# Kernel optimization log

Measured on AMD Instinct MI355X. Metric: run time of the kernel, lower is better.

The kernel has to match this reference:

```python
import jax, jax.numpy as jnp
import numpy as np

N = 50000        # nodes
E = 800000       # edges
D_IN = 128       # input feature dim (== 2*hidden)
H = 64           # hidden_dim
G = 64           # graphs in batch
BN_EPS = 1e-5


def setup_inputs() -> dict:
    key = jax.random.key(0)
    ks = jax.random.split(key, 8)
    x = jax.random.normal(ks[0], (N, D_IN), jnp.float32)
    edge_index = jax.random.randint(ks[1], (2, E), 0, N, dtype=jnp.int32)
    edge_attribute = jax.random.normal(ks[2], (E,), jnp.float32)
    batch = jnp.sort(jax.random.randint(ks[3], (N,), 0, G, dtype=jnp.int32))
    # 7 GIN layers; all first linears are [D_IN=2H -> H]
    W1 = jax.random.normal(ks[4], (7, D_IN, H), jnp.float32) * (1.0 / np.sqrt(D_IN))
    bn1_g = jnp.ones((7, H), jnp.float32)
    bn1_b = jnp.zeros((7, H), jnp.float32)
    # layers 0..5 second linear [H -> 2H] + BN
    W2 = jax.random.normal(ks[5], (6, H, 2 * H), jnp.float32) * (1.0 / np.sqrt(H))
    bn2_g = jnp.ones((6, 2 * H), jnp.float32)
    bn2_b = jnp.zeros((6, 2 * H), jnp.float32)
    # layer 6 second linear [H -> 2], no BN
    W_last = jax.random.normal(ks[6], (H, 2), jnp.float32) * (1.0 / np.sqrt(H))
    eps = jnp.zeros((7,), jnp.float32)  # train_eps=True, init 0
    return dict(x=x, edge_index=edge_index, edge_attribute=edge_attribute,
                batch=batch, W1=W1, bn1_g=bn1_g, bn1_b=bn1_b, W2=W2,
                bn2_g=bn2_g, bn2_b=bn2_b, W_last=W_last, eps=eps)


def _bn(h, g, b):
    # training-mode BatchNorm1d over node axis, biased variance
    mu = h.mean(0)
    var = h.var(0)
    return g * (h - mu) * jax.lax.rsqrt(var + BN_EPS) + b


def reference(x, edge_index, edge_attribute, batch, W1, bn1_g, bn1_b, W2,
              bn2_g, bn2_b, W_last, eps):
    src, dst = edge_index[0], edge_index[1]
    for i in range(7):
        # GIN aggregation: sum of neighbor features (edge_attribute unused)
        agg = jax.ops.segment_sum(x[src], dst, num_segments=N)
        h = (1.0 + eps[i]) * x + agg
        h = jax.nn.relu(_bn(h @ W1[i], bn1_g[i], bn1_b[i]))
        if i < 6:
            h = _bn(h @ W2[i], bn2_g[i], bn2_b[i])
        else:
            h = h @ W_last
        # F.dropout treated as identity (deterministic eval); then ReLU
        x = jax.nn.relu(h)
    # global_mean_pool over graphs
    counts = jax.ops.segment_sum(jnp.ones((N,), x.dtype), batch, num_segments=G)
    sums = jax.ops.segment_sum(x, batch, num_segments=G)
    return sums / jnp.maximum(counts, 1.0)[:, None]
```

## Files before the change

kernel.cpp:

```cpp
#include <hip/hip_runtime.h>
#include <hip/hip_fp16.h>

#define NN 50000
#define EE 800000
#define GG 64
#define BNEPS 1e-5f

typedef _Float16 f16x8 __attribute__((ext_vector_type(8)));
typedef float f32x4 __attribute__((ext_vector_type(4)));

__device__ inline float2 h2f(unsigned int u) {
    __half2 h = __builtin_bit_cast(__half2, u);
    return __half22float2(h);
}
__device__ inline unsigned int f2h(float a, float b) {
    __half2 h = __float22half2_rn(make_float2(a, b));
    return __builtin_bit_cast(unsigned int, h);
}
__device__ inline __half2 relu2(__half2 v) {
    const __half z = __float2half(0.f);
    return __halves2half2(__hmax(__low2half(v), z), __hmax(__high2half(v), z));
}


__global__ void hist_kernel(const int* __restrict__ ei, int* __restrict__ deg) {
    int e = blockIdx.x * 256 + threadIdx.x;
    if (e < EE) atomicAdd(&deg[ei[EE + e]], 1);
}

__global__ void scan1_kernel(const int* __restrict__ deg, int* __restrict__ offs,
                             int* __restrict__ bsum) {
    __shared__ int lds[1024];
    int i = blockIdx.x * 1024 + threadIdx.x;
    int v = (i < NN) ? deg[i] : 0;
    lds[threadIdx.x] = v;
    __syncthreads();
    for (int d = 1; d < 1024; d <<= 1) {
        int t = (threadIdx.x >= d) ? lds[threadIdx.x - d] : 0;
        __syncthreads();
        lds[threadIdx.x] += t;
        __syncthreads();
    }
    int incl = lds[threadIdx.x];
    if (i < NN) offs[i] = incl - v;
    if (threadIdx.x == 1023) bsum[blockIdx.x] = incl;
}

__global__ void scan3_kernel(int* __restrict__ offs, int* __restrict__ cursor,
                             const int* __restrict__ bsum) {
    __shared__ int base;
    if (threadIdx.x == 0) {
        int r = 0;
        for (int b = 0; b < (int)blockIdx.x; ++b) r += bsum[b];
        base = r;
    }
    __syncthreads();
    int i = blockIdx.x * 1024 + threadIdx.x;
    if (i < NN) {
        int o = offs[i] + base;
        offs[i] = o;
        cursor[i] = o;
    }
    if (i == 0 && blockIdx.x == 0) offs[NN] = EE;
}

__global__ void scatter_kernel(const int* __restrict__ ei, int* __restrict__ cursor,
                               unsigned short* __restrict__ srcs) {
    int e = blockIdx.x * 256 + threadIdx.x;
    if (e < EE) {
        int s = ei[e];
        int d = ei[EE + e];
        int pos = atomicAdd(&cursor[d], 1);
        srcs[pos] = (unsigned short)s;
    }
}


__global__ void cvt_kernel(const float* __restrict__ in, __half* __restrict__ out) {
    int i = blockIdx.x * 256 + threadIdx.x;
    if (i >= NN * 16) return;
    const float4* p = (const float4*)in + i * 2;
    float4 a = p[0], b = p[1];
    uint4 o;
    o.x = f2h(a.x, a.y);
    o.y = f2h(a.z, a.w);
    o.z = f2h(b.x, b.y);
    o.w = f2h(b.z, b.w);
    ((uint4*)out)[i] = o;
}


__global__ void packW_kernel(const float* __restrict__ W, __half* __restrict__ Wpk, int K,
                             int C, int layers) {
    int NKF = K / 32, NCF = C / 16;
    int per_layer = NKF * NCF * 64;
    int t = blockIdx.x * 256 + threadIdx.x;
    if (t >= layers * per_layer) return;
    int layer = t / per_layer, r = t % per_layer;
    int kf = r / (NCF * 64), r2 = r % (NCF * 64);
    int cf = r2 >> 6, l = r2 & 63;
    const float* Wl = W + (size_t)layer * K * C;
    __half* o = Wpk + ((size_t)layer * per_layer + ((size_t)(kf * NCF + cf) * 64 + l)) * 8;
    int k0 = kf * 32 + (l >> 4) * 8, c = cf * 16 + (l & 15);
#pragma unroll
    for (int j = 0; j < 8; ++j) o[j] = __float2half(Wl[(size_t)(k0 + j) * C + c]);
}


template <bool BN>
__global__ __launch_bounds__(256) void agg_kernel(const __half* __restrict__ x,
                                                  const int* __restrict__ offs,
                                                  const unsigned short* __restrict__ srcs,
                                                  const float* __restrict__ epsp, int layer,
                                                  const float* __restrict__ stats,
                                                  const float* __restrict__ bg,
                                                  const float* __restrict__ bb,
                                                  __half* __restrict__ h0) {
    __shared__ __half2 lsb2[128];
    if (BN) {
        if (threadIdx.x < 64) {
            int e = threadIdx.x;
            int p = (e & 7) * 8 + (e >> 3);
            int c0 = 2 * p, c1 = 2 * p + 1;
            float mu0 = stats[c0] * (1.0f / NN);
            float var0 = stats[128 + c0] * (1.0f / NN) - mu0 * mu0;
            float is0 = rsqrtf(var0 + BNEPS);
            float sc0 = bg[c0] * is0;
            float mu1 = stats[c1] * (1.0f / NN);
            float var1 = stats[128 + c1] * (1.0f / NN) - mu1 * mu1;
            float is1 = rsqrtf(var1 + BNEPS);
            float sc1 = bg[c1] * is1;
            lsb2[e] = __floats2half2_rn(sc0, sc1);
            lsb2[64 + e] = __floats2half2_rn(bb[c0] - mu0 * sc0, bb[c1] - mu1 * sc1);
        }
        __syncthreads();
    }
    int node = blockIdx.x * 4 + (threadIdx.x >> 6);
    if (node >= NN) return;
    int lane = threadIdx.x & 63;
    int g = lane >> 3;
    int l = lane & 7;
    __half2 sc2[8], sh2[8];
    if (BN) {
#pragma unroll
        for (int j = 0; j < 8; ++j) {
            sc2[j] = lsb2[j * 8 + l];
            sh2[j] = lsb2[64 + j * 8 + l];
        }
    }
    float acc[16];
#pragma unroll
    for (int j = 0; j < 16; ++j) acc[j] = 0.f;

    int beg = offs[node], end = offs[node + 1];
    int i0 = beg + g, i1 = i0 + 8;
    int s0 = (i0 < end) ? (int)srcs[i0] : 0;
    int s1 = (i1 < end) ? (int)srcs[i1] : 0;
    const uint4* r0 = (const uint4*)(x + (size_t)s0 * 128) + l * 2;
    const uint4* r1 = (const uint4*)(x + (size_t)s1 * 128) + l * 2;
    uint4 va = r0[0], vb = r0[1];
    uint4 wa = r1[0], wb = r1[1];
    const uint4* sp = (const uint4*)(x + (size_t)node * 128) + l * 2;
    uint4 xa, xb;
    if (g == 0) {
        xa = sp[0];
        xb = sp[1];
    }
    for (int base = beg; base + g < end; base += 8) {
        int i2 = base + 16 + g;
        int sP = (i2 < end) ? (int)srcs[i2] : 0;
        const uint4* r2 = (const uint4*)(x + (size_t)sP * 128) + l * 2;
        uint4 ua = r2[0], ub = r2[1];
#pragma unroll
        for (int j = 0; j < 8; ++j) {
            unsigned int u = (j == 0) ? va.x : (j == 1) ? va.y : (j == 2) ? va.z
                             : (j == 3) ? va.w : (j == 4) ? vb.x : (j == 5) ? vb.y
                             : (j == 6) ? vb.z : vb.w;
            __half2 hv = __builtin_bit_cast(__half2, u);
            if (BN) hv = relu2(__hfma2(hv, sc2[j], sh2[j]));
            float2 f = __half22float2(hv);
            acc[2 * j] += f.x;
            acc[2 * j + 1] += f.y;
        }
        va = wa; vb = wb;
        wa = ua; wb = ub;
    }
    float e1 = 1.0f + epsp[layer];
    if (g == 0) {
#pragma unroll
        for (int j = 0; j < 8; ++j) {
            unsigned int u = (j == 0) ? xa.x : (j == 1) ? xa.y : (j == 2) ? xa.z
                             : (j == 3) ? xa.w : (j == 4) ? xb.x : (j == 5) ? xb.y
                             : (j == 6) ? xb.z : xb.w;
            __half2 hv = __builtin_bit_cast(__half2, u);
            if (BN) hv = relu2(__hfma2(hv, sc2[j], sh2[j]));
            float2 f = __half22float2(hv);
            acc[2 * j] = fmaf(e1, f.x, acc[2 * j]);
            acc[2 * j + 1] = fmaf(e1, f.y, acc[2 * j + 1]);
        }
    }
#pragma unroll
    for (int d = 8; d < 64; d <<= 1)
#pragma unroll
        for (int j = 0; j < 16; ++j) acc[j] += __shfl_xor(acc[j], d);
    if (g == 0) {
        uint4 o0, o1;
        o0.x = f2h(acc[0], acc[1]);
        o0.y = f2h(acc[2], acc[3]);
        o0.z = f2h(acc[4], acc[5]);
        o0.w = f2h(acc[6], acc[7]);
        o1.x = f2h(acc[8], acc[9]);
        o1.y = f2h(acc[10], acc[11]);
        o1.z = f2h(acc[12], acc[13]);
        o1.w = f2h(acc[14], acc[15]);
        uint4* o = (uint4*)(h0 + (size_t)node * 128 + l * 16);
        o[0] = o0;
        o[1] = o1;
    }
}


__global__ __launch_bounds__(256) void gemm1_kernel(const __half* __restrict__ h0,
                                                    const __half* __restrict__ Wpk,
                                                    __half* __restrict__ y,
                                                    float* __restrict__ stats) {
    int lane = threadIdx.x & 63, wave = threadIdx.x >> 6, g = lane >> 4;
    f16x8 bf[4][4];
    const f16x8* wp = (const f16x8*)Wpk;
#pragma unroll
    for (int kf = 0; kf < 4; ++kf)
#pragma unroll
        for (int cf = 0; cf < 4; ++cf) bf[kf][cf] = wp[(kf * 4 + cf) * 64 + lane];
    float s[4] = {0.f, 0.f, 0.f, 0.f}, s2[4] = {0.f, 0.f, 0.f, 0.f};
    for (int tile = blockIdx.x * 4 + wave; tile < NN / 16; tile += gridDim.x * 4) {
        int node16 = tile * 16;
        f32x4 acc[4];
#pragma unroll
        for (int cf = 0; cf < 4; ++cf) acc[cf] = (f32x4){0.f, 0.f, 0.f, 0.f};
        const f16x8* xr = (const f16x8*)(h0 + (size_t)(node16 + (lane & 15)) * 128);
#pragma unroll
        for (int kf = 0; kf < 4; ++kf) {
            f16x8 af = xr[kf * 4 + g];
#pragma unroll
            for (int cf = 0; cf < 4; ++cf)
                acc[cf] =
                    __builtin_amdgcn_mfma_f32_16x16x32_f16(af, bf[kf][cf], acc[cf], 0, 0, 0);
        }
#pragma unroll
        for (int cf = 0; cf < 4; ++cf) {
#pragma unroll
            for (int r = 0; r < 4; ++r) {
                float v = acc[cf][r];
                float p = __shfl_xor(v, 1);
                if (!(lane & 1)) {
                    int node = node16 + g * 4 + r;
                    int ch = cf * 16 + (lane & 15);
                    *(unsigned int*)(y + (size_t)node * 64 + ch) = f2h(v, p);
                }
                s[cf] += v;
                s2[cf] += v * v;
            }
        }
    }
#pragma unroll
    for (int d = 16; d < 64; d <<= 1)
#pragma unroll
        for (int cf = 0; cf < 4; ++cf) {
            s[cf] += __shfl_xor(s[cf], d);
            s2[cf] += __shfl_xor(s2[cf], d);
        }
    __shared__ float lst[4][128];
    if (lane < 16) {
#pragma unroll
        for (int cf = 0; cf < 4; ++cf) {
            lst[wave][cf * 16 + lane] = s[cf];
            lst[wave][64 + cf * 16 + lane] = s2[cf];
        }
    }
    __syncthreads();
    if (threadIdx.x < 128)
        atomicAdd(&stats[threadIdx.x], lst[0][threadIdx.x] + lst[1][threadIdx.x] +
                                           lst[2][threadIdx.x] + lst[3][threadIdx.x]);
}


__global__ __launch_bounds__(256) void gemm2_kernel(const __half* __restrict__ y1,
                                                    const __half* __restrict__ Wpk,
                                                    const float* __restrict__ stats1,
                                                    const float* __restrict__ bg,
                                                    const float* __restrict__ bb,
                                                    __half* __restrict__ y2,
                                                    float* __restrict__ stats2) {
    __shared__ __half2 lsc2[32], lsh2[32];
    if (threadIdx.x < 32) {
        int p = threadIdx.x;
        int c0 = 2 * p, c1 = 2 * p + 1;
        float mu0 = stats1[c0] * (1.0f / NN);
        float var0 = stats1[64 + c0] * (1.0f / NN) - mu0 * mu0;
        float is0 = rsqrtf(var0 + BNEPS);
        float sc0 = bg[c0] * is0;
        float mu1 = stats1[c1] * (1.0f / NN);
        float var1 = stats1[64 + c1] * (1.0f / NN) - mu1 * mu1;
        float is1 = rsqrtf(var1 + BNEPS);
        float sc1 = bg[c1] * is1;
        lsc2[p] = __floats2half2_rn(sc0, sc1);
        lsh2[p] = __floats2half2_rn(bb[c0] - mu0 * sc0, bb[c1] - mu1 * sc1);
    }
    __syncthreads();
    int lane = threadIdx.x & 63, wave = threadIdx.x >> 6, g = lane >> 4;
    f16x8 bf[2][8];
    const f16x8* wp = (const f16x8*)Wpk;
#pragma unroll
    for (int kf = 0; kf < 2; ++kf)
#pragma unroll
        for (int cf = 0; cf < 8; ++cf) bf[kf][cf] = wp[(kf * 8 + cf) * 64 + lane];
    float s[8] = {0.f, 0.f, 0.f, 0.f, 0.f, 0.f, 0.f, 0.f};
    float s2[8] = {0.f, 0.f, 0.f, 0.f, 0.f, 0.f, 0.f, 0.f};
    for (int tile = blockIdx.x * 4 + wave; tile < NN / 16; tile += gridDim.x * 4) {
        int node16 = tile * 16;
        f32x4 acc[8];
#pragma unroll
        for (int cf = 0; cf < 8; ++cf) acc[cf] = (f32x4){0.f, 0.f, 0.f, 0.f};
        const f16x8* xr = (const f16x8*)(y1 + (size_t)(node16 + (lane & 15)) * 64);
#pragma unroll
        for (int kf = 0; kf < 2; ++kf) {
            f16x8 af = xr[kf * 4 + g];
            __half2* ap = (__half2*)&af;
            int p0 = kf * 16 + g * 4;
#pragma unroll
            for (int j = 0; j < 4; ++j)
                ap[j] = relu2(__hfma2(ap[j], lsc2[p0 + j], lsh2[p0 + j]));
#pragma unroll
            for (int cf = 0; cf < 8; ++cf)
                acc[cf] =
                    __builtin_amdgcn_mfma_f32_16x16x32_f16(af, bf[kf][cf], acc[cf], 0, 0, 0);
        }
#pragma unroll
        for (int cf = 0; cf < 8; ++cf) {
#pragma unroll
            for (int r = 0; r < 4; ++r) {
                float v = acc[cf][r];
                float p = __shfl_xor(v, 1);
                if (!(lane & 1)) {
                    int node = node16 + g * 4 + r;
                    int ch = cf * 16 + (lane & 15);
                    *(unsigned int*)(y2 + (size_t)node * 128 + ch) = f2h(v, p);
                }
                s[cf] += v;
                s2[cf] += v * v;
            }
        }
    }
#pragma unroll
    for (int d = 16; d < 64; d <<= 1)
#pragma unroll
        for (int cf = 0; cf < 8; ++cf) {
            s[cf] += __shfl_xor(s[cf], d);
            s2[cf] += __shfl_xor(s2[cf], d);
        }
    __shared__ float lst[4][256];
    if (lane < 16) {
#pragma unroll
        for (int cf = 0; cf < 8; ++cf) {
            lst[wave][cf * 16 + lane] = s[cf];
            lst[wave][128 + cf * 16 + lane] = s2[cf];
        }
    }
    __syncthreads();
    atomicAdd(&stats2[threadIdx.x], lst[0][threadIdx.x] + lst[1][threadIdx.x] +
                                        lst[2][threadIdx.x] + lst[3][threadIdx.x]);
}


__global__ void gemm_last_kernel(const __half* __restrict__ y1, const float* __restrict__ W,
                                 const float* __restrict__ stats1,
                                 const float* __restrict__ bg, const float* __restrict__ bb,
                                 float* __restrict__ xl) {
    __shared__ float lw[128];
    __shared__ float lsc[64], lsh[64];
    if (threadIdx.x < 128) lw[threadIdx.x] = W[threadIdx.x];
    if (threadIdx.x < 64) {
        int c = threadIdx.x;
        float mu = stats1[c] * (1.0f / NN);
        float var = stats1[64 + c] * (1.0f / NN) - mu * mu;
        float inv = rsqrtf(var + BNEPS);
        float sc = bg[c] * inv;
        lsc[c] = sc;
        lsh[c] = bb[c] - mu * sc;
    }
    __syncthreads();
    int n = blockIdx.x * 256 + threadIdx.x;
    if (n >= NN) return;
    float a0 = 0.f, a1 = 0.f;
    const uint4* row = (const uint4*)(y1 + (size_t)n * 64);
#pragma unroll
    for (int c8 = 0; c8 < 8; ++c8) {
        uint4 u = row[c8];
#pragma unroll
        for (int j = 0; j < 4; ++j) {
            unsigned int w = (j == 0) ? u.x : (j == 1) ? u.y : (j == 2) ? u.z : u.w;
            float2 f = h2f(w);
            int k = c8 * 8 + j * 2;
            float v0 = fmaxf(fmaf(f.x, lsc[k], lsh[k]), 0.f);
            float v1 = fmaxf(fmaf(f.y, lsc[k + 1], lsh[k + 1]), 0.f);
            a0 = fmaf(v0, lw[2 * k + 0], a0);
            a1 = fmaf(v0, lw[2 * k + 1], a1);
            a0 = fmaf(v1, lw[2 * k + 2], a0);
            a1 = fmaf(v1, lw[2 * k + 3], a1);
        }
    }
    xl[2 * n + 0] = fmaxf(a0, 0.f);
    xl[2 * n + 1] = fmaxf(a1, 0.f);
}


__global__ void pool_accum_kernel(const float* __restrict__ xl, const int* __restrict__ batch,
                                  float* __restrict__ pool) {
    int n = blockIdx.x * 256 + threadIdx.x;
    int lane = threadIdx.x & 63;
    int g = -1;
    float v0 = 0.f, v1 = 0.f, c = 0.f;
    if (n < NN) {
        g = batch[n];
        v0 = xl[2 * n + 0];
        v1 = xl[2 * n + 1];
        c = 1.0f;
    }
    for (int d = 1; d < 64; d <<= 1) {
        int tg = __shfl_up(g, d);
        float t0 = __shfl_up(v0, d);
        float t1 = __shfl_up(v1, d);
        float tc = __shfl_up(c, d);
        if (lane >= d && tg == g) { v0 += t0; v1 += t1; c += tc; }
    }
    int gn = __shfl_down(g, 1);
    bool lastv = (lane == 63) || (gn != g);
    if (g >= 0 && lastv) {
        atomicAdd(&pool[g * 3 + 0], v0);
        atomicAdd(&pool[g * 3 + 1], v1);
        atomicAdd(&pool[g * 3 + 2], c);
    }
}

__global__ void pool_fin_kernel(const float* __restrict__ pool, float* __restrict__ out) {
    int t = threadIdx.x;
    if (t < GG * 2) {
        int g = t >> 1, j = t & 1;
        float cnt = pool[g * 3 + 2];
        out[t] = pool[g * 3 + j] / fmaxf(cnt, 1.0f);
    }
}


extern "C" void kernel_launch(void* const* d_in, const int* in_sizes, int n_in,
                              void* d_out, int out_size, void* d_ws, size_t ws_size,
                              hipStream_t stream) {
    const float* x_in  = (const float*)d_in[0];
    const int*   ei    = (const int*)d_in[1];
    const int*   batch = (const int*)d_in[3];
    const float* W1    = (const float*)d_in[4];
    const float* bn1g  = (const float*)d_in[5];
    const float* bn1b  = (const float*)d_in[6];
    const float* W2    = (const float*)d_in[7];
    const float* bn2g  = (const float*)d_in[8];
    const float* bn2b  = (const float*)d_in[9];
    const float* Wlast = (const float*)d_in[10];
    const float* eps   = (const float*)d_in[11];
    float* out = (float*)d_out;

    char* ws = (char*)d_ws;
    size_t off = 0;
    auto alloc = [&](size_t bytes) -> char* {
        char* p = ws + off;
        off += (bytes + 255) & ~(size_t)255;
        return p;
    };
    int*   deg      = (int*)alloc((size_t)NN * 4);
    float* statsall = (float*)alloc(16 * 256 * 4);
    float* pool     = (float*)alloc((size_t)GG * 3 * 4);
    size_t zero_len = off;
    int*            offs   = (int*)alloc((size_t)(NN + 1) * 4);
    int*            cursor = (int*)alloc((size_t)NN * 4);
    int*            bsum   = (int*)alloc(64 * 4);
    unsigned short* srcs   = (unsigned short*)alloc((size_t)EE * 2);
    __half*         X16    = (__half*)alloc((size_t)NN * 128 * 2);
    __half*         A16    = (__half*)alloc((size_t)NN * 128 * 2);
    __half*         B16    = (__half*)alloc((size_t)NN * 128 * 2);
    __half*         C16    = (__half*)alloc((size_t)NN * 64 * 2);
    __half*         Wpk1   = (__half*)alloc((size_t)7 * 8192 * 2);
    __half*         Wpk2   = (__half*)alloc((size_t)6 * 8192 * 2);
    float*          xlast  = (float*)alloc((size_t)NN * 2 * 4);
    (void)ws_size; (void)n_in; (void)in_sizes; (void)out_size;

    hipMemsetAsync(ws, 0, zero_len, stream);

    hist_kernel<<<(EE + 255) / 256, 256, 0, stream>>>(ei, deg);
    scan1_kernel<<<49, 1024, 0, stream>>>(deg, offs, bsum);
    scan3_kernel<<<49, 1024, 0, stream>>>(offs, cursor, bsum);
    scatter_kernel<<<(EE + 255) / 256, 256, 0, stream>>>(ei, cursor, srcs);
    cvt_kernel<<<(NN * 16 + 255) / 256, 256, 0, stream>>>(x_in, X16);
    packW_kernel<<<(7 * 1024 + 255) / 256, 256, 0, stream>>>(W1, Wpk1, 128, 64, 7);
    packW_kernel<<<(6 * 1024 + 255) / 256, 256, 0, stream>>>(W2, Wpk2, 64, 128, 6);

    for (int i = 0; i < 7; ++i) {
        int s1 = 2 * i, s2 = 2 * i + 1;
        if (i == 0) {
            agg_kernel<false><<<(NN + 3) / 4, 256, 0, stream>>>(X16, offs, srcs, eps, i,
                                                                nullptr, nullptr, nullptr, B16);
        } else {
            agg_kernel<true><<<(NN + 3) / 4, 256, 0, stream>>>(
                A16, offs, srcs, eps, i, statsall + (2 * i - 1) * 256, bn2g + (i - 1) * 128,
                bn2b + (i - 1) * 128, B16);
        }
        gemm1_kernel<<<256, 256, 0, stream>>>(B16, Wpk1 + (size_t)i * 8192, C16,
                                              statsall + s1 * 256);
        if (i < 6) {
            gemm2_kernel<<<256, 256, 0, stream>>>(C16, Wpk2 + (size_t)i * 8192,
                                                  statsall + s1 * 256, bn1g + i * 64,
                                                  bn1b + i * 64, A16, statsall + s2 * 256);
        } else {
            gemm_last_kernel<<<(NN + 255) / 256, 256, 0, stream>>>(
                C16, Wlast, statsall + s1 * 256, bn1g + i * 64, bn1b + i * 64, xlast);
        }
    }

    pool_accum_kernel<<<(NN + 255) / 256, 256, 0, stream>>>(xlast, batch, pool);
    pool_fin_kernel<<<1, 128, 0, stream>>>(pool, out);
}
```

Baseline: 638.1 us.

## Unfuse BN2+ReLU from aggregation into separate pass; fuse pooling into last GEMM

```diff
diff --git a/kernel.cpp b/kernel.cpp
--- a/kernel.cpp
+++ b/kernel.cpp
@@ -107,47 +107,50 @@
 }
 
 
-template <bool BN>
+__global__ __launch_bounds__(256) void bnrelu_kernel(__half* __restrict__ a,
+                                                     const float* __restrict__ stats,
+                                                     const float* __restrict__ bg,
+                                                     const float* __restrict__ bb) {
+    __shared__ float lsc[128], lsh[128];
+    if (threadIdx.x < 128) {
+        int c = threadIdx.x;
+        float mu = stats[c] * (1.0f / NN);
+        float var = stats[128 + c] * (1.0f / NN) - mu * mu;
+        float inv = rsqrtf(var + BNEPS);
+        float sc = bg[c] * inv;
+        lsc[c] = sc;
+        lsh[c] = bb[c] - mu * sc;
+    }
+    __syncthreads();
+    const int total = NN * 16;
+    for (int t = blockIdx.x * 256 + threadIdx.x; t < total; t += gridDim.x * 256) {
+        uint4 u = ((const uint4*)a)[t];
+        int c0 = (t & 15) * 8;
+        unsigned int* up = &u.x;
+        uint4 o;
+        unsigned int* op = &o.x;
+#pragma unroll
+        for (int j = 0; j < 4; ++j) {
+            float2 f = h2f(up[j]);
+            f.x = fmaxf(fmaf(f.x, lsc[c0 + 2 * j], lsh[c0 + 2 * j]), 0.f);
+            f.y = fmaxf(fmaf(f.y, lsc[c0 + 2 * j + 1], lsh[c0 + 2 * j + 1]), 0.f);
+            op[j] = f2h(f.x, f.y);
+        }
+        ((uint4*)a)[t] = o;
+    }
+}
+
+
 __global__ __launch_bounds__(256) void agg_kernel(const __half* __restrict__ x,
                                                   const int* __restrict__ offs,
                                                   const unsigned short* __restrict__ srcs,
                                                   const float* __restrict__ epsp, int layer,
-                                                  const float* __restrict__ stats,
-                                                  const float* __restrict__ bg,
-                                                  const float* __restrict__ bb,
                                                   __half* __restrict__ h0) {
-    __shared__ __half2 lsb2[128];
-    if (BN) {
-        if (threadIdx.x < 64) {
-            int e = threadIdx.x;
-            int p = (e & 7) * 8 + (e >> 3);
-            int c0 = 2 * p, c1 = 2 * p + 1;
-            float mu0 = stats[c0] * (1.0f / NN);
-            float var0 = stats[128 + c0] * (1.0f / NN) - mu0 * mu0;
-            float is0 = rsqrtf(var0 + BNEPS);
-            float sc0 = bg[c0] * is0;
-            float mu1 = stats[c1] * (1.0f / NN);
-            float var1 = stats[128 + c1] * (1.0f / NN) - mu1 * mu1;
-            float is1 = rsqrtf(var1 + BNEPS);
-            float sc1 = bg[c1] * is1;
-            lsb2[e] = __floats2half2_rn(sc0, sc1);
-            lsb2[64 + e] = __floats2half2_rn(bb[c0] - mu0 * sc0, bb[c1] - mu1 * sc1);
-        }
-        __syncthreads();
-    }
     int node = blockIdx.x * 4 + (threadIdx.x >> 6);
     if (node >= NN) return;
     int lane = threadIdx.x & 63;
     int g = lane >> 3;
     int l = lane & 7;
-    __half2 sc2[8], sh2[8];
-    if (BN) {
-#pragma unroll
-        for (int j = 0; j < 8; ++j) {
-            sc2[j] = lsb2[j * 8 + l];
-            sh2[j] = lsb2[64 + j * 8 + l];
-        }
-    }
     float acc[16];
 #pragma unroll
     for (int j = 0; j < 16; ++j) acc[j] = 0.f;
@@ -176,9 +179,7 @@
             unsigned int u = (j == 0) ? va.x : (j == 1) ? va.y : (j == 2) ? va.z
                              : (j == 3) ? va.w : (j == 4) ? vb.x : (j == 5) ? vb.y
                              : (j == 6) ? vb.z : vb.w;
-            __half2 hv = __builtin_bit_cast(__half2, u);
-            if (BN) hv = relu2(__hfma2(hv, sc2[j], sh2[j]));
-            float2 f = __half22float2(hv);
+            float2 f = h2f(u);
             acc[2 * j] += f.x;
             acc[2 * j + 1] += f.y;
         }
@@ -192,9 +193,7 @@
             unsigned int u = (j == 0) ? xa.x : (j == 1) ? xa.y : (j == 2) ? xa.z
                              : (j == 3) ? xa.w : (j == 4) ? xb.x : (j == 5) ? xb.y
                              : (j == 6) ? xb.z : xb.w;
-            __half2 hv = __builtin_bit_cast(__half2, u);
-            if (BN) hv = relu2(__hfma2(hv, sc2[j], sh2[j]));
-            float2 f = __half22float2(hv);
+            float2 f = h2f(u);
             acc[2 * j] = fmaf(e1, f.x, acc[2 * j]);
             acc[2 * j + 1] = fmaf(e1, f.y, acc[2 * j + 1]);
         }
@@ -375,7 +374,7 @@
 __global__ void gemm_last_kernel(const __half* __restrict__ y1, const float* __restrict__ W,
                                  const float* __restrict__ stats1,
                                  const float* __restrict__ bg, const float* __restrict__ bb,
-                                 float* __restrict__ xl) {
+                                 const int* __restrict__ batch, float* __restrict__ pool) {
     __shared__ float lw[128];
     __shared__ float lsc[64], lsh[64];
     if (threadIdx.x < 128) lw[threadIdx.x] = W[threadIdx.x];
@@ -390,55 +389,46 @@
     }
     __syncthreads();
     int n = blockIdx.x * 256 + threadIdx.x;
-    if (n >= NN) return;
-    float a0 = 0.f, a1 = 0.f;
-    const uint4* row = (const uint4*)(y1 + (size_t)n * 64);
-#pragma unroll
-    for (int c8 = 0; c8 < 8; ++c8) {
-        uint4 u = row[c8];
-#pragma unroll
-        for (int j = 0; j < 4; ++j) {
-            unsigned int w = (j == 0) ? u.x : (j == 1) ? u.y : (j == 2) ? u.z : u.w;
-            float2 f = h2f(w);
-            int k = c8 * 8 + j * 2;
-            float v0 = fmaxf(fmaf(f.x, lsc[k], lsh[k]), 0.f);
-            float v1 = fmaxf(fmaf(f.y, lsc[k + 1], lsh[k + 1]), 0.f);
-            a0 = fmaf(v0, lw[2 * k + 0], a0);
-            a1 = fmaf(v0, lw[2 * k + 1], a1);
-            a0 = fmaf(v1, lw[2 * k + 2], a0);
-            a1 = fmaf(v1, lw[2 * k + 3], a1);
-        }
-    }
-    xl[2 * n + 0] = fmaxf(a0, 0.f);
-    xl[2 * n + 1] = fmaxf(a1, 0.f);
-}
-
-
-__global__ void pool_accum_kernel(const float* __restrict__ xl, const int* __restrict__ batch,
-                                  float* __restrict__ pool) {
-    int n = blockIdx.x * 256 + threadIdx.x;
     int lane = threadIdx.x & 63;
-    int g = -1;
-    float v0 = 0.f, v1 = 0.f, c = 0.f;
+    int gID = -1;
+    float v0 = 0.f, v1 = 0.f, cnt = 0.f;
     if (n < NN) {
-        g = batch[n];
-        v0 = xl[2 * n + 0];
-        v1 = xl[2 * n + 1];
-        c = 1.0f;
+        float a0 = 0.f, a1 = 0.f;
+        const uint4* row = (const uint4*)(y1 + (size_t)n * 64);
+#pragma unroll
+        for (int c8 = 0; c8 < 8; ++c8) {
+            uint4 u = row[c8];
+#pragma unroll
+            for (int j = 0; j < 4; ++j) {
+                unsigned int w = (j == 0) ? u.x : (j == 1) ? u.y : (j == 2) ? u.z : u.w;
+                float2 f = h2f(w);
+                int k = c8 * 8 + j * 2;
+                float t0 = fmaxf(fmaf(f.x, lsc[k], lsh[k]), 0.f);
+                float t1 = fmaxf(fmaf(f.y, lsc[k + 1], lsh[k + 1]), 0.f);
+                a0 = fmaf(t0, lw[2 * k + 0], a0);
+                a1 = fmaf(t0, lw[2 * k + 1], a1);
+                a0 = fmaf(t1, lw[2 * k + 2], a0);
+                a1 = fmaf(t1, lw[2 * k + 3], a1);
+            }
+        }
+        gID = batch[n];
+        v0 = fmaxf(a0, 0.f);
+        v1 = fmaxf(a1, 0.f);
+        cnt = 1.0f;
     }
     for (int d = 1; d < 64; d <<= 1) {
-        int tg = __shfl_up(g, d);
+        int tg = __shfl_up(gID, d);
         float t0 = __shfl_up(v0, d);
         float t1 = __shfl_up(v1, d);
-        float tc = __shfl_up(c, d);
-        if (lane >= d && tg == g) { v0 += t0; v1 += t1; c += tc; }
-    }
-    int gn = __shfl_down(g, 1);
-    bool lastv = (lane == 63) || (gn != g);
-    if (g >= 0 && lastv) {
-        atomicAdd(&pool[g * 3 + 0], v0);
-        atomicAdd(&pool[g * 3 + 1], v1);
-        atomicAdd(&pool[g * 3 + 2], c);
+        float tc = __shfl_up(cnt, d);
+        if (lane >= d && tg == gID) { v0 += t0; v1 += t1; cnt += tc; }
+    }
+    int gn = __shfl_down(gID, 1);
+    bool lastv = (lane == 63) || (gn != gID);
+    if (gID >= 0 && lastv) {
+        atomicAdd(&pool[gID * 3 + 0], v0);
+        atomicAdd(&pool[gID * 3 + 1], v1);
+        atomicAdd(&pool[gID * 3 + 2], cnt);
     }
 }
 
@@ -489,7 +479,6 @@
     __half*         C16    = (__half*)alloc((size_t)NN * 64 * 2);
     __half*         Wpk1   = (__half*)alloc((size_t)7 * 8192 * 2);
     __half*         Wpk2   = (__half*)alloc((size_t)6 * 8192 * 2);
-    float*          xlast  = (float*)alloc((size_t)NN * 2 * 4);
     (void)ws_size; (void)n_in; (void)in_sizes; (void)out_size;
 
     hipMemsetAsync(ws, 0, zero_len, stream);
@@ -504,26 +493,21 @@
 
     for (int i = 0; i < 7; ++i) {
         int s1 = 2 * i, s2 = 2 * i + 1;
-        if (i == 0) {
-            agg_kernel<false><<<(NN + 3) / 4, 256, 0, stream>>>(X16, offs, srcs, eps, i,
-                                                                nullptr, nullptr, nullptr, B16);
-        } else {
-            agg_kernel<true><<<(NN + 3) / 4, 256, 0, stream>>>(
-                A16, offs, srcs, eps, i, statsall + (2 * i - 1) * 256, bn2g + (i - 1) * 128,
-                bn2b + (i - 1) * 128, B16);
-        }
+        agg_kernel<<<(NN + 3) / 4, 256, 0, stream>>>(i == 0 ? X16 : A16, offs, srcs, eps, i,
+                                                     B16);
         gemm1_kernel<<<256, 256, 0, stream>>>(B16, Wpk1 + (size_t)i * 8192, C16,
                                               statsall + s1 * 256);
         if (i < 6) {
             gemm2_kernel<<<256, 256, 0, stream>>>(C16, Wpk2 + (size_t)i * 8192,
                                                   statsall + s1 * 256, bn1g + i * 64,
                                                   bn1b + i * 64, A16, statsall + s2 * 256);
+            bnrelu_kernel<<<2048, 256, 0, stream>>>(A16, statsall + s2 * 256,
+                                                    bn2g + i * 128, bn2b + i * 128);
         } else {
             gemm_last_kernel<<<(NN + 255) / 256, 256, 0, stream>>>(
-                C16, Wlast, statsall + s1 * 256, bn1g + i * 64, bn1b + i * 64, xlast);
-        }
-    }
-
-    pool_accum_kernel<<<(NN + 255) / 256, 256, 0, stream>>>(xlast, batch, pool);
+                C16, Wlast, statsall + s1 * 256, bn1g + i * 64, bn1b + i * 64, batch, pool);
+        }
+    }
+
     pool_fin_kernel<<<1, 128, 0, stream>>>(pool, out);
 }
```

Result: faster. 595.9 us (-6.6%).
